# Performance work log

Measured on AMD Instinct MI355X. Metric: run time of the kernel, lower is better.

Reference implementation:

```python
import jax, jax.numpy as jnp
import numpy as np

B, S, D = 2, 2048, 1024
H, KVH = 16, 4
HD = D // H          # 64
REP = H // KVH       # 4
ROPE_THETA = 10000.0


def setup_inputs() -> dict:
    key = jax.random.key(0)
    ks = jax.random.split(key, 6)
    x = jax.random.normal(ks[0], (B, S, D), dtype=jnp.float32)
    sc = 0.02
    wq = jax.random.normal(ks[1], (D, H * HD), dtype=jnp.float32) * sc
    wk = jax.random.normal(ks[2], (D, KVH * HD), dtype=jnp.float32) * sc
    wv = jax.random.normal(ks[3], (D, KVH * HD), dtype=jnp.float32) * sc
    wo = jax.random.normal(ks[4], (H * HD, D), dtype=jnp.float32) * sc
    # Llama-style rotary frequencies: freqs_cis[t, j] = exp(i * t * theta^{-2j/hd})
    inv_freq = 1.0 / (ROPE_THETA ** (jnp.arange(0, HD, 2, dtype=jnp.float32) / HD))  # [HD/2]
    t = jnp.arange(S, dtype=jnp.float32)
    ang = jnp.outer(t, inv_freq)                     # [S, HD/2]
    freqs_cos = jnp.cos(ang)
    freqs_sin = jnp.sin(ang)
    # additive causal mask [1,1,S,S]
    neg = jnp.float32(-1e9)
    mask = jnp.where(jnp.tril(jnp.ones((S, S), dtype=bool)), 0.0, neg)[None, None]
    return {"x": x, "wq": wq, "wk": wk, "wv": wv, "wo": wo,
            "freqs_cos": freqs_cos, "freqs_sin": freqs_sin, "mask": mask}


def _rope(t, cos, sin):
    # t: [B,S,h,HD]; cos/sin: [S,HD/2]; complex rotation on consecutive pairs
    tr = t[..., 0::2]
    ti = t[..., 1::2]
    c = cos[None, :, None, :]
    s = sin[None, :, None, :]
    or_ = tr * c - ti * s
    oi_ = tr * s + ti * c
    return jnp.stack([or_, oi_], axis=-1).reshape(t.shape)


def reference(x, wq, wk, wv, wo, freqs_cos, freqs_sin, mask):
    b, s, _ = x.shape
    xq = (x @ wq).reshape(b, s, H, HD)
    xk = (x @ wk).reshape(b, s, KVH, HD)
    xv = (x @ wv).reshape(b, s, KVH, HD)
    xq = _rope(xq, freqs_cos, freqs_sin)
    xk = _rope(xk, freqs_cos, freqs_sin)
    # repeat_kv: each kv head repeated REP times -> [b,s,H,HD]
    keys = jnp.repeat(xk, REP, axis=2)
    values = jnp.repeat(xv, REP, axis=2)
    q = xq.transpose(0, 2, 1, 3)      # [b,H,s,HD]
    k = keys.transpose(0, 2, 1, 3)
    v = values.transpose(0, 2, 1, 3)
    scores = jnp.einsum('bhqd,bhkd->bhqk', q, k) / jnp.sqrt(jnp.float32(HD))
    scores = scores + mask
    probs = jax.nn.softmax(scores.astype(jnp.float32), axis=-1).astype(q.dtype)
    out = jnp.einsum('bhqk,bhkd->bhqd', probs, v)
    out = out.transpose(0, 2, 1, 3).reshape(b, s, H * HD)
    return out @ wo
```

## Files before the change

kernel.cpp:

```cpp
#include <hip/hip_runtime.h>

typedef short bf8 __attribute__((ext_vector_type(8)));
typedef float f32x4 __attribute__((ext_vector_type(4)));
typedef float f32x16 __attribute__((ext_vector_type(16)));
typedef int i32x4 __attribute__((ext_vector_type(4)));

__device__ __forceinline__ ushort f2b(float f) {
  unsigned x = __builtin_bit_cast(unsigned, f);
  unsigned r = (x + 0x7fffu + ((x >> 16) & 1u)) >> 16;
  return (ushort)r;
}
__device__ __forceinline__ float b2f(ushort u) {
  unsigned x = ((unsigned)u) << 16;
  return __builtin_bit_cast(float, x);
}

__device__ __forceinline__ f32x4 mfma16(bf8 a, bf8 b, f32x4 c) {
  return __builtin_amdgcn_mfma_f32_16x16x32_bf16(a, b, c, 0, 0, 0);
}
__device__ __forceinline__ f32x16 mfma32(bf8 a, bf8 b, f32x16 c) {
  return __builtin_amdgcn_mfma_f32_32x32x16_bf16(a, b, c, 0, 0, 0);
}

__device__ __forceinline__ float fexp2(float x) {
#if __has_builtin(__builtin_amdgcn_exp2f)
  return __builtin_amdgcn_exp2f(x);
#else
  return exp2f(x);
#endif
}

__device__ __forceinline__ uint cvtpk(float lo, float hi_) {
  uint r;
  asm("v_cvt_pk_bf16_f32 %0, %1, %2" : "=v"(r) : "v"(lo), "v"(hi_));
  return r;
}
__device__ __forceinline__ void plswap(uint& a, uint& b) {
  asm("v_permlane32_swap_b32 %0, %1" : "+v"(a), "+v"(b));
}

__device__ __forceinline__ void gload16(const ushort* g, ushort* l) {
  __builtin_amdgcn_global_load_lds(
      (const __attribute__((address_space(1))) void*)g,
      (__attribute__((address_space(3))) void*)l, 16, 0, 0);
}

__global__ __launch_bounds__(256) void prep1(
    const float* __restrict__ x, const float* __restrict__ wq,
    const float* __restrict__ wk, const float* __restrict__ wv,
    const float* __restrict__ wo, ushort* __restrict__ xb,
    ushort* __restrict__ wqkvT, ushort* __restrict__ woT) {
  __shared__ float tile[32][33];
  const int bid = blockIdx.x;
  if (bid < 4096) {
    const int i = (bid * 256 + threadIdx.x) * 4;
    float4 v = *(const float4*)(x + i);
    ushort4 o;
    o.x = f2b(v.x); o.y = f2b(v.y); o.z = f2b(v.z); o.w = f2b(v.w);
    *(ushort4*)(xb + i) = o;
    return;
  }
  int t = bid - 4096;
  const float* src;
  ushort* dst;
  int N;
  if (t < 1024) {
    src = wq; dst = wqkvT; N = 1024;
  } else if (t < 1280) {
    src = wk; dst = wqkvT + 1024 * 1024; N = 256; t -= 1024;
  } else if (t < 1536) {
    src = wv; dst = wqkvT + 1280 * 1024; N = 256; t -= 1280;
  } else {
    src = wo; dst = woT; N = 1024; t -= 1536;
  }
  const int kx = (t & 31) * 32, nx = (t >> 5) * 32;
  const int tx = threadIdx.x & 31, ty = threadIdx.x >> 5;
#pragma unroll
  for (int i = ty; i < 32; i += 8)
    tile[i][tx] = src[(size_t)(kx + i) * N + nx + tx];
  __syncthreads();
#pragma unroll
  for (int i = ty; i < 32; i += 8)
    dst[(size_t)(nx + i) * 1024 + kx + tx] = f2b(tile[tx][i]);
}

template <bool OUT_BF16>
__global__ __launch_bounds__(256) void gemm_bt(const ushort* __restrict__ A,
                                               const ushort* __restrict__ Bt,
                                               void* __restrict__ Cv, int M,
                                               int N, int K) {
  __shared__ ushort aL[64 * 64];
  __shared__ ushort bL[128 * 64];
  const int tid = threadIdx.x;
  const int wid = tid >> 6, lane = tid & 63;
  const int l15 = lane & 15, l4 = lane >> 4;
  const int bm = blockIdx.y * 64, bn = blockIdx.x * 128;
  const int wr = (wid & 1) * 32, wc = (wid >> 1) * 64;
  f32x4 acc[2][4] = {};
  for (int kb = 0; kb < K; kb += 64) {
    __syncthreads();
#pragma unroll
    for (int i = 0; i < 2; ++i) {
      const int e = (i * 256 + tid) * 8;
      const int r = e >> 6, c = e & 63;
      gload16(A + (size_t)(bm + r) * K + kb + c, &aL[i * 2048 + wid * 512]);
    }
#pragma unroll
    for (int i = 0; i < 4; ++i) {
      const int e = (i * 256 + tid) * 8;
      const int r = e >> 6, c = e & 63;
      gload16(Bt + (size_t)(bn + r) * K + kb + c, &bL[i * 2048 + wid * 512]);
    }
    asm volatile("s_waitcnt vmcnt(0)" ::: "memory");
    __syncthreads();
    bf8 af[2][2], bfr[4][2];
#pragma unroll
    for (int i = 0; i < 2; ++i)
#pragma unroll
      for (int kk = 0; kk < 2; ++kk)
        af[i][kk] =
            *(const bf8*)&aL[(wr + i * 16 + l15) * 64 + kk * 32 + l4 * 8];
#pragma unroll
    for (int j = 0; j < 4; ++j)
#pragma unroll
      for (int kk = 0; kk < 2; ++kk)
        bfr[j][kk] =
            *(const bf8*)&bL[(wc + j * 16 + l15) * 64 + kk * 32 + l4 * 8];
#pragma unroll
    for (int kk = 0; kk < 2; ++kk)
#pragma unroll
      for (int i = 0; i < 2; ++i)
#pragma unroll
        for (int j = 0; j < 4; ++j)
          acc[i][j] = mfma16(af[i][kk], bfr[j][kk], acc[i][j]);
  }
#pragma unroll
  for (int i = 0; i < 2; ++i)
#pragma unroll
    for (int j = 0; j < 4; ++j)
#pragma unroll
      for (int r = 0; r < 4; ++r) {
        const size_t row = bm + wr + i * 16 + l4 * 4 + r;
        const size_t col = bn + wc + j * 16 + l15;
        if constexpr (OUT_BF16)
          ((ushort*)Cv)[row * N + col] = f2b(acc[i][j][r]);
        else
          ((float*)Cv)[row * N + col] = acc[i][j][r];
      }
}

__global__ __launch_bounds__(256) void prep2(const ushort* __restrict__ qkv,
                                             const float* __restrict__ fc,
                                             const float* __restrict__ fs,
                                             ushort* __restrict__ qh,
                                             ushort* __restrict__ kh,
                                             ushort* __restrict__ vT) {
  __shared__ ushort tile[64][65];
  if (blockIdx.x < 10240) {
    const int idx = blockIdx.x * 256 + threadIdx.x;
    const int u = idx % 640;
    const int m = idx / 640;
    const int s = m & 2047, b = m >> 11;
    int col, j;
    if (u < 512) {
      j = u & 31;
      col = (u >> 5) * 64 + 2 * j;
    } else {
      j = (u - 512) & 31;
      col = 1024 + ((u - 512) >> 5) * 64 + 2 * j;
    }
    const uint pr = *(const uint*)(qkv + (size_t)m * 1536 + col);
    const float tr = b2f((ushort)(pr & 0xffff));
    const float ti = b2f((ushort)(pr >> 16));
    const float c = fc[s * 32 + j], sn = fs[s * 32 + j];
    float orr = tr * c - ti * sn;
    float oi = tr * sn + ti * c;
    if (u < 512) {
      orr *= 0.18033688f;
      oi *= 0.18033688f;
      const uint w = (uint)f2b(orr) | ((uint)f2b(oi) << 16);
      *(uint*)(qh + ((size_t)(b * 16 + (u >> 5)) * 2048 + s) * 64 + 2 * j) = w;
    } else {
      const uint w = (uint)f2b(orr) | ((uint)f2b(oi) << 16);
      const int kv = (u - 512) >> 5;
      *(uint*)(kh + ((size_t)(b * 4 + kv) * 2048 + s) * 64 + 2 * j) = w;
    }
    return;
  }
  const int id = blockIdx.x - 10240;
  const int st = id & 31, kv = (id >> 5) & 3, b = id >> 7;
  const int tid = threadIdx.x;
  for (int e = tid; e < 4096; e += 256) {
    const int r = e >> 6, c = e & 63;
    tile[r][c] =
        qkv[(size_t)(b * 2048 + st * 64 + r) * 1536 + 1280 + kv * 64 + c];
  }
  __syncthreads();
  for (int e = tid; e < 4096; e += 256) {
    const int d = e >> 6, c = e & 63;
    vT[((size_t)(b * 4 + kv) * 64 + d) * 2048 + st * 64 + c] = tile[c][d];
  }
}


#define MCONST 12.0f

__device__ __forceinline__ void astep2(const bf8 (&kfA)[4], const bf8 (&kfB)[4],
                                       const bf8 (&vfA)[4], const bf8 (&vfB)[4],
                                       const bf8 (&qf)[4], f32x16& o0,
                                       f32x16& o1, float& l, int k0, int qg,
                                       bool maskt, int hi) {
  f32x16 s0 = {}, s1 = {};
  __builtin_amdgcn_s_setprio(1);
#pragma unroll
  for (int ks = 0; ks < 4; ++ks) s0 = mfma32(kfA[ks], qf[ks], s0);
#pragma unroll
  for (int ks = 0; ks < 4; ++ks) s1 = mfma32(kfB[ks], qf[ks], s1);
  __builtin_amdgcn_s_setprio(0);
  if (maskt) {
#pragma unroll
    for (int r = 0; r < 16; ++r) {
      const int key = k0 + (r & 3) + 8 * (r >> 2) + 4 * hi;
      if (key > qg) s0[r] = -1e30f;
      if (key + 32 > qg) s1[r] = -1e30f;
    }
  }
  float t[16];
#pragma unroll
  for (int r = 0; r < 16; ++r) {
    s0[r] = fexp2(s0[r] - MCONST);
    s1[r] = fexp2(s1[r] - MCONST);
    t[r] = s0[r] + s1[r];
  }
#pragma unroll
  for (int st = 8; st > 0; st >>= 1)
#pragma unroll
    for (int r = 0; r < st; ++r) t[r] += t[r + st];
  l += t[0] + __shfl_xor(t[0], 32);
  bf8 pa[4];
  {
    uint a0 = cvtpk(s0[0], s0[1]), a1 = cvtpk(s0[2], s0[3]);
    uint b0 = cvtpk(s0[4], s0[5]), b1 = cvtpk(s0[6], s0[7]);
    plswap(a0, b0);
    plswap(a1, b1);
    i32x4 w = {(int)a0, (int)a1, (int)b0, (int)b1};
    pa[0] = __builtin_bit_cast(bf8, w);
    uint c0 = cvtpk(s0[8], s0[9]), c1 = cvtpk(s0[10], s0[11]);
    uint d0 = cvtpk(s0[12], s0[13]), d1 = cvtpk(s0[14], s0[15]);
    plswap(c0, d0);
    plswap(c1, d1);
    i32x4 w2 = {(int)c0, (int)c1, (int)d0, (int)d1};
    pa[1] = __builtin_bit_cast(bf8, w2);
  }
  {
    uint a0 = cvtpk(s1[0], s1[1]), a1 = cvtpk(s1[2], s1[3]);
    uint b0 = cvtpk(s1[4], s1[5]), b1 = cvtpk(s1[6], s1[7]);
    plswap(a0, b0);
    plswap(a1, b1);
    i32x4 w = {(int)a0, (int)a1, (int)b0, (int)b1};
    pa[2] = __builtin_bit_cast(bf8, w);
    uint c0 = cvtpk(s1[8], s1[9]), c1 = cvtpk(s1[10], s1[11]);
    uint d0 = cvtpk(s1[12], s1[13]), d1 = cvtpk(s1[14], s1[15]);
    plswap(c0, d0);
    plswap(c1, d1);
    i32x4 w2 = {(int)c0, (int)c1, (int)d0, (int)d1};
    pa[3] = __builtin_bit_cast(bf8, w2);
  }
  __builtin_amdgcn_s_setprio(1);
#pragma unroll
  for (int ks = 0; ks < 4; ++ks) o0 = mfma32(vfA[ks], pa[ks], o0);
#pragma unroll
  for (int ks = 0; ks < 4; ++ks) o1 = mfma32(vfB[ks], pa[ks], o1);
  __builtin_amdgcn_s_setprio(0);
}

__device__ __forceinline__ void tile_out(ushort* ow, const f32x16& o0,
                                         const f32x16& o1, float l, int b,
                                         int h, int qw, int l31, int hi,
                                         int lane, ushort* ao) {
  const float inv = 1.0f / l;
#pragma unroll
  for (int dt = 0; dt < 2; ++dt)
#pragma unroll
    for (int rq = 0; rq < 4; ++rq) {
      const f32x16& ac = dt ? o1 : o0;
      uint2 w;
      w.x = (uint)f2b(ac[rq * 4 + 0] * inv) |
            ((uint)f2b(ac[rq * 4 + 1] * inv) << 16);
      w.y = (uint)f2b(ac[rq * 4 + 2] * inv) |
            ((uint)f2b(ac[rq * 4 + 3] * inv) << 16);
      const int d = dt * 32 + 8 * rq + 4 * hi;
      *(uint2*)&ow[l31 * 66 + d] = w;
    }
  asm volatile("s_waitcnt lgkmcnt(0)" ::: "memory");
  __builtin_amdgcn_sched_barrier(0);
  const int rrow = lane >> 4;
  const int rcol = (lane & 15) * 4;
  const size_t gbase = ((size_t)b * 2048 + qw) * 1024 + h * 64;
#pragma unroll
  for (int i = 0; i < 8; ++i) {
    const int rw = i * 4 + rrow;
    uint2 v = *(const uint2*)&ow[rw * 66 + rcol];
    *(uint2*)&ao[gbase + (size_t)rw * 1024 + rcol] = v;
  }
}

__global__ __launch_bounds__(256) void attn_fwd(const ushort* __restrict__ qh,
                                                const ushort* __restrict__ kh,
                                                const ushort* __restrict__ vT,
                                                ushort* __restrict__ ao) {
  __shared__ ushort kls[4096];
  __shared__ ushort vls[4096];
  __shared__ ushort olds[4][2176];
  const int tid = threadIdx.x;
  const int wid = tid >> 6, lane = tid & 63;
  const int l31 = lane & 31, hi = lane >> 5;
  const int gid = blockIdx.x;
  const int bk = gid & 7;
  const int b = bk >> 2, kv = bk & 3;
  const int rest = gid >> 3;
  const int p = rest & 31, half = rest >> 5;
  const int t = half ? (63 - p) : p;
  const int h = kv * 4 + wid;
  const int n = (32 * t + 95) >> 6;
  const int qg = t * 32 + l31;

  const ushort* kbase = kh + (size_t)(b * 4 + kv) * 2048 * 64;
  const ushort* vbase = vT + (size_t)(b * 4 + kv) * 64 * 2048;

  auto stage = [&](int k0) {
#pragma unroll
    for (int jj2 = 0; jj2 < 2; ++jj2) {
      const int jj = wid + jj2 * 4;
      const int i = jj * 64 + lane;
      const int r = i >> 3, s = i & 7;
      const int sw = (s ^ (r & 7)) << 3;
      gload16(kbase + (size_t)(k0 + r) * 64 + sw, kls + jj * 512);
      gload16(vbase + (size_t)r * 2048 + k0 + sw, vls + jj * 512);
    }
  };

  stage(0);

  bf8 qf[4];
  {
    const ushort* qb = qh + ((size_t)(b * 16 + h) * 2048 + qg) * 64 + hi * 8;
#pragma unroll
    for (int ks = 0; ks < 4; ++ks) qf[ks] = *(const bf8*)(qb + ks * 16);
  }

  f32x16 o0 = {}, o1 = {};
  float l = 0.f;
  const int sw0 = l31 & 7;

  for (int it = 0; it < n; ++it) {
    asm volatile("s_waitcnt vmcnt(0)" ::: "memory");
    __builtin_amdgcn_s_barrier();
    asm volatile("" ::: "memory");
    bf8 kfA[4], kfB[4], vfA[4], vfB[4];
#pragma unroll
    for (int ks = 0; ks < 4; ++ks) {
      const int c2 = 2 * ks + hi;
      const int off = (c2 ^ sw0) << 3;
      kfA[ks] = *(const bf8*)&kls[l31 * 64 + off];
      kfB[ks] = *(const bf8*)&kls[(32 + l31) * 64 + off];
      vfA[ks] = *(const bf8*)&vls[l31 * 64 + off];
      vfB[ks] = *(const bf8*)&vls[(32 + l31) * 64 + off];
    }
    asm volatile("s_waitcnt lgkmcnt(0)" ::: "memory");
    __builtin_amdgcn_sched_barrier(0);
    __builtin_amdgcn_s_barrier();
    if (it + 1 < n) stage((it + 1) * 64);
    astep2(kfA, kfB, vfA, vfB, qf, o0, o1, l, it * 64, qg, it == n - 1, hi);
  }
  tile_out(olds[wid], o0, o1, l, b, h, t * 32, l31, hi, lane, ao);
}

extern "C" void kernel_launch(void* const* d_in, const int* in_sizes, int n_in,
                              void* d_out, int out_size, void* d_ws,
                              size_t ws_size, hipStream_t stream) {
  (void)in_sizes; (void)n_in; (void)out_size; (void)ws_size;
  const float* x = (const float*)d_in[0];
  const float* wq = (const float*)d_in[1];
  const float* wk = (const float*)d_in[2];
  const float* wv = (const float*)d_in[3];
  const float* wo = (const float*)d_in[4];
  const float* fc = (const float*)d_in[5];
  const float* fs = (const float*)d_in[6];
  float* out = (float*)d_out;

  ushort* xb = (ushort*)d_ws;
  ushort* wqkvT = xb + 4194304;
  ushort* woT = wqkvT + 1572864;
  ushort* qkv = woT + 1048576;
  ushort* qh = qkv + 6291456;
  ushort* kh = qh + 4194304;
  ushort* vTb = kh + 1048576;
  ushort* ao = vTb + 1048576;

  prep1<<<6656, 256, 0, stream>>>(x, wq, wk, wv, wo, xb, wqkvT, woT);
  gemm_bt<true><<<dim3(12, 64), 256, 0, stream>>>(xb, wqkvT, qkv, 4096, 1536, 1024);
  prep2<<<10496, 256, 0, stream>>>(qkv, fc, fs, qh, kh, vTb);
  attn_fwd<<<512, 256, 0, stream>>>(qh, kh, vTb, ao);
  gemm_bt<false><<<dim3(8, 64), 256, 0, stream>>>(ao, woT, out, 4096, 1024, 1024);
}
```

Before: 112.9 us.

## Triple-buffer K/V tiles in attention with two-ahead prefetch

Replaces the single-buffered K/V LDS staging with a three-slot ring buffer. Loads are issued two tiles ahead and the loop waits with vmcnt(4) instead of vmcnt(0), and the second barrier per iteration is removed so global loads overlap more compute. Block-to-tile mapping also changes to interleave query tiles (t = 2u+half, n = u+1). Redundant dummy loads at the tail and higher LDS usage (about 48KB for K/V) may reduce occupancy.

Result: slower. 121.2 us (+7.3%).

```diff
diff --git a/kernel.cpp b/kernel.cpp
--- a/kernel.cpp
+++ b/kernel.cpp
@@ -309,8 +309,8 @@
                                                 const ushort* __restrict__ kh,
                                                 const ushort* __restrict__ vT,
                                                 ushort* __restrict__ ao) {
-  __shared__ ushort kls[4096];
-  __shared__ ushort vls[4096];
+  __shared__ ushort kls[3][4096];
+  __shared__ ushort vls[3][4096];
   __shared__ ushort olds[4][2176];
   const int tid = threadIdx.x;
   const int wid = tid >> 6, lane = tid & 63;
@@ -319,28 +319,30 @@
   const int bk = gid & 7;
   const int b = bk >> 2, kv = bk & 3;
   const int rest = gid >> 3;
-  const int p = rest & 31, half = rest >> 5;
-  const int t = half ? (63 - p) : p;
+  const int u = rest & 31, half = rest >> 5;
+  const int t = 2 * u + half;
   const int h = kv * 4 + wid;
-  const int n = (32 * t + 95) >> 6;
+  const int n = u + 1;
   const int qg = t * 32 + l31;
 
   const ushort* kbase = kh + (size_t)(b * 4 + kv) * 2048 * 64;
   const ushort* vbase = vT + (size_t)(b * 4 + kv) * 64 * 2048;
 
-  auto stage = [&](int k0) {
+  auto stage = [&](int j, int buf) {
+    const int k0 = j * 64;
 #pragma unroll
     for (int jj2 = 0; jj2 < 2; ++jj2) {
       const int jj = wid + jj2 * 4;
       const int i = jj * 64 + lane;
       const int r = i >> 3, s = i & 7;
       const int sw = (s ^ (r & 7)) << 3;
-      gload16(kbase + (size_t)(k0 + r) * 64 + sw, kls + jj * 512);
-      gload16(vbase + (size_t)r * 2048 + k0 + sw, vls + jj * 512);
+      gload16(kbase + (size_t)(k0 + r) * 64 + sw, kls[buf] + jj * 512);
+      gload16(vbase + (size_t)r * 2048 + k0 + sw, vls[buf] + jj * 512);
     }
   };
 
-  stage(0);
+  stage(0, 0);
+  stage(n > 1 ? 1 : 0, 1);
 
   bf8 qf[4];
   {
@@ -354,23 +356,27 @@
   const int sw0 = l31 & 7;
 
   for (int it = 0; it < n; ++it) {
-    asm volatile("s_waitcnt vmcnt(0)" ::: "memory");
+    asm volatile("s_waitcnt vmcnt(4)" ::: "memory");
     __builtin_amdgcn_s_barrier();
     asm volatile("" ::: "memory");
+    {
+      const int nx = (it + 2 < n) ? (it + 2) : (n - 1);
+      stage(nx, (it + 2) % 3);
+    }
+    const ushort* kb_l = kls[it % 3];
+    const ushort* vb_l = vls[it % 3];
     bf8 kfA[4], kfB[4], vfA[4], vfB[4];
 #pragma unroll
     for (int ks = 0; ks < 4; ++ks) {
       const int c2 = 2 * ks + hi;
       const int off = (c2 ^ sw0) << 3;
-      kfA[ks] = *(const bf8*)&kls[l31 * 64 + off];
-      kfB[ks] = *(const bf8*)&kls[(32 + l31) * 64 + off];
-      vfA[ks] = *(const bf8*)&vls[l31 * 64 + off];
-      vfB[ks] = *(const bf8*)&vls[(32 + l31) * 64 + off];
+      kfA[ks] = *(const bf8*)&kb_l[l31 * 64 + off];
+      kfB[ks] = *(const bf8*)&kb_l[(32 + l31) * 64 + off];
+      vfA[ks] = *(const bf8*)&vb_l[l31 * 64 + off];
+      vfB[ks] = *(const bf8*)&vb_l[(32 + l31) * 64 + off];
     }
     asm volatile("s_waitcnt lgkmcnt(0)" ::: "memory");
     __builtin_amdgcn_sched_barrier(0);
-    __builtin_amdgcn_s_barrier();
-    if (it + 1 < n) stage((it + 1) * 64);
     astep2(kfA, kfB, vfA, vfB, qf, o0, o1, l, it * 64, qg, it == n - 1, hi);
   }
   tile_out(olds[wid], o0, o1, l, b, h, t * 32, l31, hi, lane, ao);
```

## Process two KV tiles per barrier iteration in attention loop

Applied to the files above, without the earlier changes.

The attention kernel now stages two 64-key K/V tiles into a doubled LDS buffer per outer iteration and runs two compute steps per barrier pair. This halves the number of vmcnt waits and workgroup barriers and gives each prefetch more compute to hide behind. It doubles the LDS for K/V and raises fragment register pressure, which may reduce occupancy. When the tile count is odd, the second slot re-loads the last tile and its compute step is skipped.

After: 106.6 us. 1.06x faster.

```diff
diff --git a/kernel.cpp b/kernel.cpp
--- a/kernel.cpp
+++ b/kernel.cpp
@@ -309,8 +309,8 @@
                                                 const ushort* __restrict__ kh,
                                                 const ushort* __restrict__ vT,
                                                 ushort* __restrict__ ao) {
-  __shared__ ushort kls[4096];
-  __shared__ ushort vls[4096];
+  __shared__ ushort kls[2][4096];
+  __shared__ ushort vls[2][4096];
   __shared__ ushort olds[4][2176];
   const int tid = threadIdx.x;
   const int wid = tid >> 6, lane = tid & 63;
@@ -323,24 +323,32 @@
   const int t = half ? (63 - p) : p;
   const int h = kv * 4 + wid;
   const int n = (32 * t + 95) >> 6;
+  const int nss = (n + 1) >> 1;
   const int qg = t * 32 + l31;
 
   const ushort* kbase = kh + (size_t)(b * 4 + kv) * 2048 * 64;
   const ushort* vbase = vT + (size_t)(b * 4 + kv) * 64 * 2048;
 
-  auto stage = [&](int k0) {
+  auto stageTile = [&](int j, int hf) {
+    const int k0 = j * 64;
 #pragma unroll
     for (int jj2 = 0; jj2 < 2; ++jj2) {
       const int jj = wid + jj2 * 4;
       const int i = jj * 64 + lane;
       const int r = i >> 3, s = i & 7;
       const int sw = (s ^ (r & 7)) << 3;
-      gload16(kbase + (size_t)(k0 + r) * 64 + sw, kls + jj * 512);
-      gload16(vbase + (size_t)r * 2048 + k0 + sw, vls + jj * 512);
+      gload16(kbase + (size_t)(k0 + r) * 64 + sw, kls[hf] + jj * 512);
+      gload16(vbase + (size_t)r * 2048 + k0 + sw, vls[hf] + jj * 512);
     }
   };
-
-  stage(0);
+  auto stageSS = [&](int ss) {
+    const int j0 = 2 * ss;
+    const int j1 = (2 * ss + 1 < n) ? (2 * ss + 1) : (n - 1);
+    stageTile(j0, 0);
+    stageTile(j1, 1);
+  };
+
+  stageSS(0);
 
   bf8 qf[4];
   {
@@ -353,25 +361,32 @@
   float l = 0.f;
   const int sw0 = l31 & 7;
 
-  for (int it = 0; it < n; ++it) {
+  for (int ss = 0; ss < nss; ++ss) {
     asm volatile("s_waitcnt vmcnt(0)" ::: "memory");
     __builtin_amdgcn_s_barrier();
     asm volatile("" ::: "memory");
-    bf8 kfA[4], kfB[4], vfA[4], vfB[4];
-#pragma unroll
-    for (int ks = 0; ks < 4; ++ks) {
-      const int c2 = 2 * ks + hi;
-      const int off = (c2 ^ sw0) << 3;
-      kfA[ks] = *(const bf8*)&kls[l31 * 64 + off];
-      kfB[ks] = *(const bf8*)&kls[(32 + l31) * 64 + off];
-      vfA[ks] = *(const bf8*)&vls[l31 * 64 + off];
-      vfB[ks] = *(const bf8*)&vls[(32 + l31) * 64 + off];
-    }
+    bf8 kfA[2][4], kfB[2][4], vfA[2][4], vfB[2][4];
+#pragma unroll
+    for (int hf = 0; hf < 2; ++hf)
+#pragma unroll
+      for (int ks = 0; ks < 4; ++ks) {
+        const int c2 = 2 * ks + hi;
+        const int off = (c2 ^ sw0) << 3;
+        kfA[hf][ks] = *(const bf8*)&kls[hf][l31 * 64 + off];
+        kfB[hf][ks] = *(const bf8*)&kls[hf][(32 + l31) * 64 + off];
+        vfA[hf][ks] = *(const bf8*)&vls[hf][l31 * 64 + off];
+        vfB[hf][ks] = *(const bf8*)&vls[hf][(32 + l31) * 64 + off];
+      }
     asm volatile("s_waitcnt lgkmcnt(0)" ::: "memory");
     __builtin_amdgcn_sched_barrier(0);
     __builtin_amdgcn_s_barrier();
-    if (it + 1 < n) stage((it + 1) * 64);
-    astep2(kfA, kfB, vfA, vfB, qf, o0, o1, l, it * 64, qg, it == n - 1, hi);
+    if (ss + 1 < nss) stageSS(ss + 1);
+    const int j0 = 2 * ss, j1 = 2 * ss + 1;
+    astep2(kfA[0], kfB[0], vfA[0], vfB[0], qf, o0, o1, l, j0 * 64, qg,
+           j0 == n - 1, hi);
+    if (j1 < n)
+      astep2(kfA[1], kfB[1], vfA[1], vfB[1], qf, o0, o1, l, j1 * 64, qg,
+             j1 == n - 1, hi);
   }
   tile_out(olds[wid], o0, o1, l, b, h, t * 32, l31, hi, lane, ao);
 }
```
